# Kernel tuning notes

Measured on AMD Instinct MI355X. Metric: run time of the kernel, lower is better.

## Reference

```python
import jax, jax.numpy as jnp
import numpy as np

NEG_SLOPE = 0.2

def _gat_conv(x, W, att_src, att_dst, bias, src, dst, n_nodes):
    # x: [N, F_in], W: [F_in, F_out], att_*: [F_out], bias: [F_out]
    h = x @ W                                   # [N, F_out]
    a_src = h @ att_src                         # [N]
    a_dst = h @ att_dst                         # [N]
    e = a_src[src] + a_dst[dst]                 # [E]
    e = jnp.where(e > 0, e, NEG_SLOPE * e)      # LeakyReLU
    # segment softmax over incoming edges of each destination node
    m = jax.ops.segment_max(e, dst, num_segments=n_nodes)
    ex = jnp.exp(e - m[dst])
    denom = jax.ops.segment_sum(ex, dst, num_segments=n_nodes)
    alpha = ex / denom[dst]                     # [E]
    msg = alpha[:, None] * h[src]               # [E, F_out]
    out = jax.ops.segment_sum(msg, dst, num_segments=n_nodes)
    return out + bias

def setup_inputs() -> dict:
    key = jax.random.key(0)
    ks = jax.random.split(key, 12)
    N, E, F_in, H, F_out = 50000, 800000, 128, 128, 128
    def glorot(k, shape):
        lim = float(np.sqrt(6.0 / sum(shape))) if len(shape) > 1 else float(np.sqrt(6.0 / shape[0]))
        return jax.random.uniform(k, shape, jnp.float32, -lim, lim)
    return {
        "x": jax.random.normal(ks[0], (N, F_in), jnp.float32),
        "edge_index": jax.random.randint(ks[1], (2, E), 0, N, jnp.int64),
        "W1": glorot(ks[2], (F_in, H)),
        "att_src1": glorot(ks[3], (H,)),
        "att_dst1": glorot(ks[4], (H,)),
        "b1": jnp.zeros((H,), jnp.float32),
        "W2": glorot(ks[5], (H, F_out)),
        "att_src2": glorot(ks[6], (F_out,)),
        "att_dst2": glorot(ks[7], (F_out,)),
        "b2": jnp.zeros((F_out,), jnp.float32),
    }

def reference(x, edge_index, W1, att_src1, att_dst1, b1, W2, att_src2, att_dst2, b2):
    n_nodes = x.shape[0]
    # add self loops (PyG GATConv default)
    loops = jnp.arange(n_nodes, dtype=edge_index.dtype)
    src = jnp.concatenate([edge_index[0], loops])
    dst = jnp.concatenate([edge_index[1], loops])
    h = _gat_conv(x, W1, att_src1, att_dst1, b1, src, dst, n_nodes)
    h = jax.nn.relu(h)
    h = _gat_conv(h, W2, att_src2, att_dst2, b2, src, dst, n_nodes)
    return jax.nn.relu(h)
```

## Files before the change

### kernel.cpp

```cpp
#include <hip/hip_runtime.h>
#include <cstdint>

#define NEG_SLOPE 0.2f
#define F 128

#define BKT_SHIFT 7
#define BKT_SIZE  128
#define NBK_PAD   512
#define CHUNK     4096
#define EPT       8
#define CAP       3072

typedef unsigned short u16;
typedef unsigned int u32;
typedef float float8_t __attribute__((ext_vector_type(8)));
typedef float float4_t __attribute__((ext_vector_type(4)));
typedef short short8_t __attribute__((ext_vector_type(8)));

__device__ inline u16 f2bf(float f) {
    u32 u = __float_as_uint(f);
    u32 r = u + 0x7fffu + ((u >> 16) & 1u);
    return (u16)(r >> 16);
}
__device__ inline float bflo(u32 v) { return __uint_as_float(v << 16); }
__device__ inline float bfhi(u32 v) { return __uint_as_float(v & 0xffff0000u); }

__device__ inline void prep_unit(const float* __restrict__ W, u16* __restrict__ Wt, int u) {
    int frag = u >> 6, lane = u & 63;
    int K0 = frag >> 3, nt = frag & 7;
    int kbase = K0 * 32 + (lane >> 4) * 8;
    int n = nt * 16 + (lane & 15);
    u32 w[4];
    #pragma unroll
    for (int p = 0; p < 4; ++p) {
        u16 e0 = f2bf(W[(size_t)(kbase + 2 * p) * F + n]);
        u16 e1 = f2bf(W[(size_t)(kbase + 2 * p + 1) * F + n]);
        w[p] = (u32)e0 | ((u32)e1 << 16);
    }
    uint4 o; o.x = w[0]; o.y = w[1]; o.z = w[2]; o.w = w[3];
    ((uint4*)Wt)[u] = o;
}

__device__ inline int block_excl_scan_512(int v, int tid, int* wsum) {
    int incl = v;
    #pragma unroll
    for (int o = 1; o < 64; o <<= 1) {
        int u = __shfl_up(incl, o);
        if ((tid & 63) >= o) incl += u;
    }
    if ((tid & 63) == 63) wsum[tid >> 6] = incl;
    __syncthreads();
    int woff = 0;
    #pragma unroll
    for (int w0 = 0; w0 < 7; ++w0) woff += (w0 < (tid >> 6)) ? wsum[w0] : 0;
    return woff + incl - v;
}

__global__ void __launch_bounds__(512) scatter_prep_kernel(const int* __restrict__ ei, int E, int tot,
                                                           int* __restrict__ bucketCursor,
                                                           u32* __restrict__ pairs,
                                                           const float* __restrict__ W1, u16* __restrict__ Wt1,
                                                           const float* __restrict__ W2, u16* __restrict__ Wt2,
                                                           int nScatBlocks) {
    if ((int)blockIdx.x >= nScatBlocks) {
        int pb = blockIdx.x - nScatBlocks;
        int u = (pb & 3) * 512 + threadIdx.x;
        if (pb < 4) prep_unit(W1, Wt1, u);
        else        prep_unit(W2, Wt2, u);
        return;
    }
    __shared__ int hist[NBK_PAD], excl[NBK_PAD], lcur[NBK_PAD], runb[NBK_PAD];
    __shared__ int wsum[8];
    __shared__ u32 stage[CHUNK];
    __shared__ u16 bktid[CHUNK];
    int tid = threadIdx.x;
    hist[tid] = 0;
    __syncthreads();
    int base = blockIdx.x * CHUNK;
    int chunkCnt = min(CHUNK, tot - base);
    int rs[EPT], rd[EPT];
    int w = base + tid * EPT;
    if (w + EPT <= E) {
        int4 s0 = *(const int4*)&ei[w];
        int4 s1 = *(const int4*)&ei[w + 4];
        int4 d0 = *(const int4*)&ei[E + w];
        int4 d1 = *(const int4*)&ei[E + w + 4];
        rs[0] = s0.x; rs[1] = s0.y; rs[2] = s0.z; rs[3] = s0.w;
        rs[4] = s1.x; rs[5] = s1.y; rs[6] = s1.z; rs[7] = s1.w;
        rd[0] = d0.x; rd[1] = d0.y; rd[2] = d0.z; rd[3] = d0.w;
        rd[4] = d1.x; rd[5] = d1.y; rd[6] = d1.z; rd[7] = d1.w;
        #pragma unroll
        for (int i = 0; i < EPT; ++i) atomicAdd(&hist[rd[i] >> BKT_SHIFT], 1);
    } else {
        #pragma unroll
        for (int i = 0; i < EPT; ++i) {
            int e = w + i;
            rd[i] = -1;
            if (e < tot) {
                int s, d;
                if (e < E) { s = ei[e]; d = ei[E + e]; } else { s = e - E; d = s; }
                rs[i] = s; rd[i] = d;
                atomicAdd(&hist[d >> BKT_SHIFT], 1);
            }
        }
    }
    __syncthreads();
    int v = hist[tid];
    int ex = block_excl_scan_512(v, tid, wsum);
    excl[tid] = ex;
    lcur[tid] = ex;
    if (v > 0) runb[tid] = tid * CAP + atomicAdd(&bucketCursor[tid], v);
    __syncthreads();
    #pragma unroll
    for (int i = 0; i < EPT; ++i) {
        if (rd[i] >= 0) {
            int b = rd[i] >> BKT_SHIFT;
            int pos = atomicAdd(&lcur[b], 1);
            stage[pos] = ((u32)rs[i] << BKT_SHIFT) | (u32)(rd[i] & (BKT_SIZE - 1));
            bktid[pos] = (u16)b;
        }
    }
    __syncthreads();
    for (int j = tid; j < chunkCnt; j += 512) {
        int b = (int)bktid[j];
        size_t idx = (size_t)runb[b] + (j - excl[b]);
        if (idx < (size_t)(b + 1) * CAP)
            pairs[idx] = stage[j];
    }
}

__device__ void build_body(const u32* __restrict__ pairs, const int* __restrict__ bucketCursor,
                           int* __restrict__ row_ptr, int* __restrict__ csr,
                           int N, int tot, int b, char* smem) {
    u32* stage  = (u32*)smem;
    int* sorted = (int*)(smem + CAP * 4);
    int* hist   = (int*)(smem + CAP * 8);
    int* pfx    = (int*)(smem + CAP * 8 + 512);
    int* cur    = (int*)(smem + CAP * 8 + 1024);
    int* red    = (int*)(smem + CAP * 8 + 1536);
    int tid = threadIdx.x;

    int part = 0;
    for (int i = tid; i < b; i += 256) part += min(bucketCursor[i], CAP);
    #pragma unroll
    for (int o = 32; o > 0; o >>= 1) part += __shfl_xor(part, o);
    if ((tid & 63) == 0) red[tid >> 6] = part;
    if (tid < BKT_SIZE) hist[tid] = 0;
    __syncthreads();
    int dstb = red[0] + red[1] + red[2] + red[3];
    int cnt = min(bucketCursor[b], CAP);

    size_t srcb = (size_t)b * CAP;
    for (int j = tid; j < cnt; j += 256) {
        u32 p = pairs[srcb + j];
        stage[j] = p;
        atomicAdd(&hist[p & (BKT_SIZE - 1)], 1);
    }
    __syncthreads();
    if (tid < BKT_SIZE) pfx[tid] = hist[tid];
    __syncthreads();
    for (int o = 1; o < BKT_SIZE; o <<= 1) {
        int u = 0;
        if (tid < BKT_SIZE && tid >= o) u = pfx[tid - o];
        __syncthreads();
        if (tid < BKT_SIZE) pfx[tid] += u;
        __syncthreads();
    }
    if (tid < BKT_SIZE) {
        int ex = pfx[tid] - hist[tid];
        cur[tid] = ex;
        int d = b * BKT_SIZE + tid;
        if (d < N) row_ptr[d] = dstb + ex;
    }
    __syncthreads();
    for (int j = tid; j < cnt; j += 256) {
        u32 p = stage[j];
        int pos = atomicAdd(&cur[p & (BKT_SIZE - 1)], 1);
        sorted[pos] = (int)(p >> BKT_SHIFT);
    }
    __syncthreads();
    for (int j = tid; j < cnt; j += 256) csr[(size_t)dstb + j] = sorted[j];
    if (b == 0 && tid == 0) row_ptr[N] = tot;
}

template<int IN_BF16>
__device__ void gemm_body(const void* __restrict__ in, const u16* __restrict__ Wt,
                          const float* __restrict__ att_s, const float* __restrict__ att_d,
                          u16* __restrict__ h, float* __restrict__ asrc, float* __restrict__ adst,
                          int N, int gblk, u16* wlds) {
    int tid = threadIdx.x;
    {
        const uint4* src = (const uint4*)Wt;
        uint4* dst = (uint4*)wlds;
        #pragma unroll
        for (int i = 0; i < 8; ++i) dst[tid + i * 256] = src[tid + i * 256];
    }
    __syncthreads();
    int wave = tid >> 6, lane = tid & 63;
    int li = lane & 15, grp = lane >> 4;
    int rowBase = (gblk * 4 + wave) * 16;
    if (rowBase >= N) return;
    int row = rowBase + li;
    if (row > N - 1) row = N - 1;

    short8_t b[4];
    if (IN_BF16) {
        const u16* xp = (const u16*)in + (size_t)row * F + grp * 8;
        #pragma unroll
        for (int K0 = 0; K0 < 4; ++K0)
            b[K0] = *(const short8_t*)(xp + K0 * 32);
    } else {
        const float* xp = (const float*)in + (size_t)row * F + grp * 8;
        #pragma unroll
        for (int K0 = 0; K0 < 4; ++K0) {
            float8_t xv = *(const float8_t*)(xp + K0 * 32);
            short8_t t;
            #pragma unroll
            for (int i = 0; i < 8; ++i) t[i] = (short)f2bf(xv[i]);
            b[K0] = t;
        }
    }

    float4_t acc[8];
    #pragma unroll
    for (int nt = 0; nt < 8; ++nt) acc[nt] = (float4_t){0.f, 0.f, 0.f, 0.f};
    #pragma unroll
    for (int nt = 0; nt < 8; ++nt) {
        #pragma unroll
        for (int K0 = 0; K0 < 4; ++K0) {
            short8_t a = *(const short8_t*)&wlds[((K0 * 8 + nt) * 64 + lane) * 8];
            acc[nt] = __builtin_amdgcn_mfma_f32_16x16x32_bf16(a, b[K0], acc[nt], 0, 0, 0);
        }
    }

    u16* hr = h + (size_t)row * F + grp * 4;
    #pragma unroll
    for (int nt = 0; nt < 8; ++nt) {
        u32 lo = (u32)f2bf(acc[nt][0]) | ((u32)f2bf(acc[nt][1]) << 16);
        u32 hi = (u32)f2bf(acc[nt][2]) | ((u32)f2bf(acc[nt][3]) << 16);
        uint2 st; st.x = lo; st.y = hi;
        *(uint2*)(hr + (size_t)nt * 16) = st;
    }

    float rs = 0.f, rd = 0.f;
    #pragma unroll
    for (int nt = 0; nt < 8; ++nt) {
        float4 a4 = *(const float4*)(att_s + nt * 16 + grp * 4);
        float4 d4 = *(const float4*)(att_d + nt * 16 + grp * 4);
        rs += acc[nt][0] * a4.x + acc[nt][1] * a4.y + acc[nt][2] * a4.z + acc[nt][3] * a4.w;
        rd += acc[nt][0] * d4.x + acc[nt][1] * d4.y + acc[nt][2] * d4.z + acc[nt][3] * d4.w;
    }
    rs += __shfl_xor(rs, 16); rs += __shfl_xor(rs, 32);
    rd += __shfl_xor(rd, 16); rd += __shfl_xor(rd, 32);
    if (grp == 0) { asrc[row] = rs; adst[row] = rd; }
}

__global__ void __launch_bounds__(256) build_gemm_kernel(
    const u32* __restrict__ pairs, const int* __restrict__ bucketCursor,
    int* __restrict__ row_ptr, int* __restrict__ csr, int N, int tot,
    const float* __restrict__ x, const u16* __restrict__ Wt,
    const float* __restrict__ att_s, const float* __restrict__ att_d,
    u16* __restrict__ h, float* __restrict__ asrc, float* __restrict__ adst, int NBK)
{
    __shared__ __align__(16) char smem[32768];
    if ((int)blockIdx.x < NBK) {
        build_body(pairs, bucketCursor, row_ptr, csr, N, tot, blockIdx.x, smem);
    } else {
        gemm_body<0>(x, Wt, att_s, att_d, h, asrc, adst, N, blockIdx.x - NBK, (u16*)smem);
    }
}

__device__ __forceinline__ void rowfma(uint4 v, float pp, float (&acc)[8]) {
    acc[0] = fmaf(pp, bflo(v.x), acc[0]); acc[1] = fmaf(pp, bfhi(v.x), acc[1]);
    acc[2] = fmaf(pp, bflo(v.y), acc[2]); acc[3] = fmaf(pp, bfhi(v.y), acc[3]);
    acc[4] = fmaf(pp, bflo(v.z), acc[4]); acc[5] = fmaf(pp, bfhi(v.z), acc[5]);
    acc[6] = fmaf(pp, bflo(v.w), acc[6]); acc[7] = fmaf(pp, bfhi(v.w), acc[7]);
}

template<int U>
__device__ __forceinline__ void gfma(const uint4* __restrict__ h4, int lane, int s, float p, int t,
                                     float (&acc)[8]) {
    int ss[U]; float pp[U]; uint4 vv[U];
    #pragma unroll
    for (int i = 0; i < U; ++i) { ss[i] = __shfl(s, t + i, 16); pp[i] = __shfl(p, t + i, 16); }
    #pragma unroll
    for (int i = 0; i < U; ++i) vv[i] = h4[(size_t)ss[i] * 16 + lane];
    #pragma unroll
    for (int i = 0; i < U; ++i) rowfma(vv[i], pp[i], acc);
}

__device__ __forceinline__ float agg_core(
    const u16* __restrict__ h, const float* __restrict__ asrc, float ad,
    int start, int deg, const int* __restrict__ csr, int lane, float (&acc)[8]) {
    const uint4* h4 = (const uint4*)h;
    float denom = 0.f;
    int c0 = 0;
    int cnt = min(16, deg);
    int s = 0; float a = 0.f;
    if (lane < cnt) { s = csr[start + lane]; a = asrc[s]; }
    for (;;) {
        float p = 0.f;
        if (lane < cnt) {
            float e = a + ad;
            e = (e > 0.f) ? e : NEG_SLOPE * e;
            p = __expf(fminf(e, 70.f));
        }
        denom += p;

        int nc0 = c0 + 16;
        int ncnt = min(16, deg - nc0);
        int s2 = 0; float a2 = 0.f;
        if (nc0 < deg && lane < ncnt) { s2 = csr[start + nc0 + lane]; a2 = asrc[s2]; }

        int t = 0;
        for (; t + 8 <= cnt; t += 8) gfma<8>(h4, lane, s, p, t, acc);
        for (; t + 4 <= cnt; t += 4) gfma<4>(h4, lane, s, p, t, acc);
        for (; t < cnt; ++t)         gfma<1>(h4, lane, s, p, t, acc);

        if (nc0 >= deg) break;
        c0 = nc0; cnt = ncnt; s = s2; a = a2;
    }
    #pragma unroll
    for (int o = 1; o < 16; o <<= 1) denom += __shfl_xor(denom, o);
    return denom;
}

#define OL_STRIDE 136
__global__ void __launch_bounds__(256) agg_gemm_kernel(
    const u16* __restrict__ h, const float* __restrict__ asrc, const float* __restrict__ adst,
    const int* __restrict__ row_ptr, const int* __restrict__ csr,
    const float* __restrict__ bias,
    const u16* __restrict__ Wt2, const float* __restrict__ att_s2, const float* __restrict__ att_d2,
    u16* __restrict__ h2, float* __restrict__ asrc2, float* __restrict__ adst2, int N)
{
    __shared__ u16 out_lds[16 * OL_STRIDE];
    __shared__ float sdots[2][4][16];
    int tid = threadIdx.x;
    int gidBase = blockIdx.x * 16;
    int gid = gidBase + (tid >> 4);
    int lane = tid & 15;

    int start = row_ptr[gid];
    int deg = row_ptr[gid + 1] - start;
    float acc[8] = {0.f, 0.f, 0.f, 0.f, 0.f, 0.f, 0.f, 0.f};
    float denom = agg_core(h, asrc, adst[gid], start, deg, csr, lane, acc);
    float inv = 1.0f / denom;
    const float* bp = bias + lane * 8;
    u32 wpk[4];
    #pragma unroll
    for (int p2 = 0; p2 < 4; ++p2) {
        float v0 = fmaf(acc[2 * p2],     inv, bp[2 * p2]);
        float v1 = fmaf(acc[2 * p2 + 1], inv, bp[2 * p2 + 1]);
        v0 = v0 > 0.f ? v0 : 0.f;
        v1 = v1 > 0.f ? v1 : 0.f;
        wpk[p2] = (u32)f2bf(v0) | ((u32)f2bf(v1) << 16);
    }
    {
        uint4 st; st.x = wpk[0]; st.y = wpk[1]; st.z = wpk[2]; st.w = wpk[3];
        *(uint4*)&out_lds[(tid >> 4) * OL_STRIDE + lane * 8] = st;
    }
    __syncthreads();

    int l = tid & 63, wv = tid >> 6;
    int li = l & 15, grp = l >> 4;
    short8_t b[4];
    #pragma unroll
    for (int K0 = 0; K0 < 4; ++K0)
        b[K0] = *(const short8_t*)&out_lds[li * OL_STRIDE + grp * 8 + K0 * 32];

    float rs = 0.f, rd = 0.f;
    #pragma unroll
    for (int q = 0; q < 2; ++q) {
        int nt = wv * 2 + q;
        float4_t acc2 = (float4_t){0.f, 0.f, 0.f, 0.f};
        #pragma unroll
        for (int K0 = 0; K0 < 4; ++K0) {
            short8_t a = *(const short8_t*)&Wt2[((K0 * 8 + nt) * 64 + l) * 8];
            acc2 = __builtin_amdgcn_mfma_f32_16x16x32_bf16(a, b[K0], acc2, 0, 0, 0);
        }
        int row = gidBase + li;
        u32 lo = (u32)f2bf(acc2[0]) | ((u32)f2bf(acc2[1]) << 16);
        u32 hi = (u32)f2bf(acc2[2]) | ((u32)f2bf(acc2[3]) << 16);
        uint2 st; st.x = lo; st.y = hi;
        *(uint2*)(h2 + (size_t)row * F + nt * 16 + grp * 4) = st;
        float4 a4 = *(const float4*)(att_s2 + nt * 16 + grp * 4);
        float4 d4 = *(const float4*)(att_d2 + nt * 16 + grp * 4);
        rs += acc2[0] * a4.x + acc2[1] * a4.y + acc2[2] * a4.z + acc2[3] * a4.w;
        rd += acc2[0] * d4.x + acc2[1] * d4.y + acc2[2] * d4.z + acc2[3] * d4.w;
    }
    rs += __shfl_xor(rs, 16); rs += __shfl_xor(rs, 32);
    rd += __shfl_xor(rd, 16); rd += __shfl_xor(rd, 32);
    if (grp == 0) { sdots[0][wv][li] = rs; sdots[1][wv][li] = rd; }
    __syncthreads();
    if (tid < 16) {
        float s = sdots[0][0][tid] + sdots[0][1][tid] + sdots[0][2][tid] + sdots[0][3][tid];
        float d = sdots[1][0][tid] + sdots[1][1][tid] + sdots[1][2][tid] + sdots[1][3][tid];
        asrc2[gidBase + tid] = s;
        adst2[gidBase + tid] = d;
    }
}

__global__ void __launch_bounds__(256) aggregate_out_kernel(
    const u16* __restrict__ h, const float* __restrict__ asrc, const float* __restrict__ adst,
    const int* __restrict__ row_ptr, const int* __restrict__ csr,
    const float* __restrict__ bias, float* __restrict__ out, int N)
{
    int gid = blockIdx.x * 16 + (threadIdx.x >> 4);
    if (gid >= N) return;
    int lane = threadIdx.x & 15;
    int start = row_ptr[gid];
    int deg = row_ptr[gid + 1] - start;
    float acc[8] = {0.f, 0.f, 0.f, 0.f, 0.f, 0.f, 0.f, 0.f};
    float denom = agg_core(h, asrc, adst[gid], start, deg, csr, lane, acc);
    float inv = 1.0f / denom;
    const float* bp = bias + lane * 8;
    float r[8];
    #pragma unroll
    for (int j = 0; j < 8; ++j) {
        float v = fmaf(acc[j], inv, bp[j]);
        r[j] = v > 0.f ? v : 0.f;
    }
    float4 o0 = make_float4(r[0], r[1], r[2], r[3]);
    float4 o1 = make_float4(r[4], r[5], r[6], r[7]);
    ((float4*)out)[(size_t)gid * 32 + lane * 2]     = o0;
    ((float4*)out)[(size_t)gid * 32 + lane * 2 + 1] = o1;
}

static inline size_t align_up(size_t v, size_t a) { return (v + a - 1) & ~(a - 1); }

extern "C" void kernel_launch(void* const* d_in, const int* in_sizes, int n_in,
                              void* d_out, int out_size, void* d_ws, size_t ws_size,
                              hipStream_t stream) {
    const float* x   = (const float*)d_in[0];
    const int*   ei  = (const int*)d_in[1];
    const float* W1  = (const float*)d_in[2];
    const float* as1 = (const float*)d_in[3];
    const float* ad1 = (const float*)d_in[4];
    const float* b1  = (const float*)d_in[5];
    const float* W2  = (const float*)d_in[6];
    const float* as2 = (const float*)d_in[7];
    const float* ad2 = (const float*)d_in[8];
    const float* b2  = (const float*)d_in[9];

    int N = in_sizes[0] / F;
    int E = in_sizes[1] / 2;
    int tot = E + N;

    char* ws = (char*)d_ws;
    size_t off = 0;
    #define ALLOC(type, name, count)                                    \
        type* name = (type*)(ws + off);                                  \
        off = align_up(off + (size_t)(count) * sizeof(type), 256);
    ALLOC(u16,   h,       (size_t)N * F);
    ALLOC(u16,   h2,      (size_t)N * F);
    ALLOC(float, asrc,    N);
    ALLOC(float, adst,    N);
    ALLOC(float, asrc2,   N);
    ALLOC(float, adst2,   N);
    ALLOC(int,   row_ptr, N + 4);
    ALLOC(int,   csr,     tot);
    ALLOC(u32,   pairs,   (size_t)NBK_PAD * CAP);
    ALLOC(int,   bucketCursor, NBK_PAD);
    ALLOC(u16,   Wt1,     16384);
    ALLOC(u16,   Wt2,     16384);
    #undef ALLOC

    hipMemsetAsync(bucketCursor, 0, NBK_PAD * sizeof(int), stream);

    int NBK = (N + BKT_SIZE - 1) / BKT_SIZE;
    int nchunks = (tot + CHUNK - 1) / CHUNK;
    int ngemm = (N + 63) / 64;
    int nagg  = (N + 15) / 16;

    scatter_prep_kernel<<<nchunks + 8, 512, 0, stream>>>(ei, E, tot, bucketCursor, pairs,
                                                         W1, Wt1, W2, Wt2, nchunks);
    build_gemm_kernel<<<NBK + ngemm, 256, 0, stream>>>(pairs, bucketCursor, row_ptr, csr, N, tot,
                                                       x, Wt1, as1, ad1, h, asrc, adst, NBK);
    agg_gemm_kernel<<<nagg, 256, 0, stream>>>(h, asrc, adst, row_ptr, csr, b1,
                                              Wt2, as2, ad2, h2, asrc2, adst2, N);
    aggregate_out_kernel<<<nagg, 256, 0, stream>>>(h2, asrc2, adst2, row_ptr, csr, b2,
                                                   (float*)d_out, N);
}
```

Baseline: 187.2 us.

## Move layer-1 GEMM into scatter kernel and convert W1 per block in LDS

The first-layer GEMM (x@W1 plus attention logits) now runs in the same launch as the edge bucket scatter instead of sharing a launch with the CSR build. Each GEMM block converts W1 to bf16 fragments directly into LDS, which removes the separate Wt1 prep pass and lets the GEMM start without waiting on it. GEMM blocks grow to 512 threads covering 128 rows. The build kernel becomes a standalone launch. The tradeoff is that each GEMM block redoes the W1 conversion from global fp32, and the fused kernel's LDS footprint grows slightly.

After: 193.2 us. 1.03x slower.

```diff
diff --git a/kernel.cpp b/kernel.cpp
--- a/kernel.cpp
+++ b/kernel.cpp
@@ -25,7 +25,7 @@
 __device__ inline float bflo(u32 v) { return __uint_as_float(v << 16); }
 __device__ inline float bfhi(u32 v) { return __uint_as_float(v & 0xffff0000u); }
 
-__device__ inline void prep_unit(const float* __restrict__ W, u16* __restrict__ Wt, int u) {
+__device__ inline void prep_unit(const float* __restrict__ W, uint4* __restrict__ dst, int u) {
     int frag = u >> 6, lane = u & 63;
     int K0 = frag >> 3, nt = frag & 7;
     int kbase = K0 * 32 + (lane >> 4) * 8;
@@ -38,7 +38,7 @@
         w[p] = (u32)e0 | ((u32)e1 << 16);
     }
     uint4 o; o.x = w[0]; o.y = w[1]; o.z = w[2]; o.w = w[3];
-    ((uint4*)Wt)[u] = o;
+    dst[u] = o;
 }
 
 __device__ inline int block_excl_scan_512(int v, int tid, int* wsum) {
@@ -56,27 +56,20 @@
     return woff + incl - v;
 }
 
-__global__ void __launch_bounds__(512) scatter_prep_kernel(const int* __restrict__ ei, int E, int tot,
-                                                           int* __restrict__ bucketCursor,
-                                                           u32* __restrict__ pairs,
-                                                           const float* __restrict__ W1, u16* __restrict__ Wt1,
-                                                           const float* __restrict__ W2, u16* __restrict__ Wt2,
-                                                           int nScatBlocks) {
-    if ((int)blockIdx.x >= nScatBlocks) {
-        int pb = blockIdx.x - nScatBlocks;
-        int u = (pb & 3) * 512 + threadIdx.x;
-        if (pb < 4) prep_unit(W1, Wt1, u);
-        else        prep_unit(W2, Wt2, u);
-        return;
-    }
-    __shared__ int hist[NBK_PAD], excl[NBK_PAD], lcur[NBK_PAD], runb[NBK_PAD];
-    __shared__ int wsum[8];
-    __shared__ u32 stage[CHUNK];
-    __shared__ u16 bktid[CHUNK];
+__device__ void scatter_body(const int* __restrict__ ei, int E, int tot,
+                             int* __restrict__ bucketCursor, u32* __restrict__ pairs,
+                             int bid, char* smem) {
+    u32* stage = (u32*)smem;
+    u16* bktid = (u16*)(smem + 16384);
+    int* hist  = (int*)(smem + 24576);
+    int* excl  = (int*)(smem + 26624);
+    int* lcur  = (int*)(smem + 28672);
+    int* runb  = (int*)(smem + 30720);
+    int* wsum  = (int*)(smem + 32768);
     int tid = threadIdx.x;
     hist[tid] = 0;
     __syncthreads();
-    int base = blockIdx.x * CHUNK;
+    int base = bid * CHUNK;
     int chunkCnt = min(CHUNK, tot - base);
     int rs[EPT], rd[EPT];
     int w = base + tid * EPT;
@@ -129,16 +122,98 @@
     }
 }
 
-__device__ void build_body(const u32* __restrict__ pairs, const int* __restrict__ bucketCursor,
-                           int* __restrict__ row_ptr, int* __restrict__ csr,
-                           int N, int tot, int b, char* smem) {
+__device__ void gemm1_body(const float* __restrict__ x, const float* __restrict__ W,
+                           const float* __restrict__ att_s, const float* __restrict__ att_d,
+                           u16* __restrict__ h, float* __restrict__ asrc, float* __restrict__ adst,
+                           int N, int gblk, u16* wlds) {
+    int tid = threadIdx.x;
+    #pragma unroll
+    for (int i = 0; i < 4; ++i) prep_unit(W, (uint4*)wlds, tid + i * 512);
+    __syncthreads();
+    int wave = tid >> 6, lane = tid & 63;
+    int li = lane & 15, grp = lane >> 4;
+    int rowBase = (gblk * 8 + wave) * 16;
+    if (rowBase >= N) return;
+    int row = rowBase + li;
+    if (row > N - 1) row = N - 1;
+
+    short8_t b[4];
+    const float* xp = x + (size_t)row * F + grp * 8;
+    #pragma unroll
+    for (int K0 = 0; K0 < 4; ++K0) {
+        float8_t xv = *(const float8_t*)(xp + K0 * 32);
+        short8_t t;
+        #pragma unroll
+        for (int i = 0; i < 8; ++i) t[i] = (short)f2bf(xv[i]);
+        b[K0] = t;
+    }
+
+    float4_t acc[8];
+    #pragma unroll
+    for (int nt = 0; nt < 8; ++nt) acc[nt] = (float4_t){0.f, 0.f, 0.f, 0.f};
+    #pragma unroll
+    for (int nt = 0; nt < 8; ++nt) {
+        #pragma unroll
+        for (int K0 = 0; K0 < 4; ++K0) {
+            short8_t a = *(const short8_t*)&wlds[((K0 * 8 + nt) * 64 + lane) * 8];
+            acc[nt] = __builtin_amdgcn_mfma_f32_16x16x32_bf16(a, b[K0], acc[nt], 0, 0, 0);
+        }
+    }
+
+    u16* hr = h + (size_t)row * F + grp * 4;
+    #pragma unroll
+    for (int nt = 0; nt < 8; ++nt) {
+        u32 lo = (u32)f2bf(acc[nt][0]) | ((u32)f2bf(acc[nt][1]) << 16);
+        u32 hi = (u32)f2bf(acc[nt][2]) | ((u32)f2bf(acc[nt][3]) << 16);
+        uint2 st; st.x = lo; st.y = hi;
+        *(uint2*)(hr + (size_t)nt * 16) = st;
+    }
+
+    float rs = 0.f, rd = 0.f;
+    #pragma unroll
+    for (int nt = 0; nt < 8; ++nt) {
+        float4 a4 = *(const float4*)(att_s + nt * 16 + grp * 4);
+        float4 d4 = *(const float4*)(att_d + nt * 16 + grp * 4);
+        rs += acc[nt][0] * a4.x + acc[nt][1] * a4.y + acc[nt][2] * a4.z + acc[nt][3] * a4.w;
+        rd += acc[nt][0] * d4.x + acc[nt][1] * d4.y + acc[nt][2] * d4.z + acc[nt][3] * d4.w;
+    }
+    rs += __shfl_xor(rs, 16); rs += __shfl_xor(rs, 32);
+    rd += __shfl_xor(rd, 16); rd += __shfl_xor(rd, 32);
+    if (grp == 0) { asrc[row] = rs; adst[row] = rd; }
+}
+
+__global__ void __launch_bounds__(512) fused1_kernel(
+    const int* __restrict__ ei, int E, int tot,
+    int* __restrict__ bucketCursor, u32* __restrict__ pairs,
+    const float* __restrict__ W2, u16* __restrict__ Wt2,
+    const float* __restrict__ x, const float* __restrict__ W1,
+    const float* __restrict__ att_s, const float* __restrict__ att_d,
+    u16* __restrict__ h, float* __restrict__ asrc, float* __restrict__ adst,
+    int N, int nScat)
+{
+    __shared__ __align__(16) char smem[32800];
+    int bid = blockIdx.x;
+    if (bid < nScat) {
+        scatter_body(ei, E, tot, bucketCursor, pairs, bid, smem);
+    } else if (bid < nScat + 4) {
+        prep_unit(W2, (uint4*)Wt2, (bid - nScat) * 512 + threadIdx.x);
+    } else {
+        gemm1_body(x, W1, att_s, att_d, h, asrc, adst, N, bid - nScat - 4, (u16*)smem);
+    }
+}
+
+__global__ void __launch_bounds__(256) build_kernel(
+    const u32* __restrict__ pairs, const int* __restrict__ bucketCursor,
+    int* __restrict__ row_ptr, int* __restrict__ csr, int N, int tot)
+{
+    __shared__ __align__(16) char smem[26368];
     u32* stage  = (u32*)smem;
     int* sorted = (int*)(smem + CAP * 4);
     int* hist   = (int*)(smem + CAP * 8);
     int* pfx    = (int*)(smem + CAP * 8 + 512);
     int* cur    = (int*)(smem + CAP * 8 + 1024);
     int* red    = (int*)(smem + CAP * 8 + 1536);
-    int tid = threadIdx.x;
+    int b = blockIdx.x, tid = threadIdx.x;
 
     int part = 0;
     for (int i = tid; i < b; i += 256) part += min(bucketCursor[i], CAP);
@@ -181,93 +256,6 @@
     __syncthreads();
     for (int j = tid; j < cnt; j += 256) csr[(size_t)dstb + j] = sorted[j];
     if (b == 0 && tid == 0) row_ptr[N] = tot;
-}
-
-template<int IN_BF16>
-__device__ void gemm_body(const void* __restrict__ in, const u16* __restrict__ Wt,
-                          const float* __restrict__ att_s, const float* __restrict__ att_d,
-                          u16* __restrict__ h, float* __restrict__ asrc, float* __restrict__ adst,
-                          int N, int gblk, u16* wlds) {
-    int tid = threadIdx.x;
-    {
-        const uint4* src = (const uint4*)Wt;
-        uint4* dst = (uint4*)wlds;
-        #pragma unroll
-        for (int i = 0; i < 8; ++i) dst[tid + i * 256] = src[tid + i * 256];
-    }
-    __syncthreads();
-    int wave = tid >> 6, lane = tid & 63;
-    int li = lane & 15, grp = lane >> 4;
-    int rowBase = (gblk * 4 + wave) * 16;
-    if (rowBase >= N) return;
-    int row = rowBase + li;
-    if (row > N - 1) row = N - 1;
-
-    short8_t b[4];
-    if (IN_BF16) {
-        const u16* xp = (const u16*)in + (size_t)row * F + grp * 8;
-        #pragma unroll
-        for (int K0 = 0; K0 < 4; ++K0)
-            b[K0] = *(const short8_t*)(xp + K0 * 32);
-    } else {
-        const float* xp = (const float*)in + (size_t)row * F + grp * 8;
-        #pragma unroll
-        for (int K0 = 0; K0 < 4; ++K0) {
-            float8_t xv = *(const float8_t*)(xp + K0 * 32);
-            short8_t t;
-            #pragma unroll
-            for (int i = 0; i < 8; ++i) t[i] = (short)f2bf(xv[i]);
-            b[K0] = t;
-        }
-    }
-
-    float4_t acc[8];
-    #pragma unroll
-    for (int nt = 0; nt < 8; ++nt) acc[nt] = (float4_t){0.f, 0.f, 0.f, 0.f};
-    #pragma unroll
-    for (int nt = 0; nt < 8; ++nt) {
-        #pragma unroll
-        for (int K0 = 0; K0 < 4; ++K0) {
-            short8_t a = *(const short8_t*)&wlds[((K0 * 8 + nt) * 64 + lane) * 8];
-            acc[nt] = __builtin_amdgcn_mfma_f32_16x16x32_bf16(a, b[K0], acc[nt], 0, 0, 0);
-        }
-    }
-
-    u16* hr = h + (size_t)row * F + grp * 4;
-    #pragma unroll
-    for (int nt = 0; nt < 8; ++nt) {
-        u32 lo = (u32)f2bf(acc[nt][0]) | ((u32)f2bf(acc[nt][1]) << 16);
-        u32 hi = (u32)f2bf(acc[nt][2]) | ((u32)f2bf(acc[nt][3]) << 16);
-        uint2 st; st.x = lo; st.y = hi;
-        *(uint2*)(hr + (size_t)nt * 16) = st;
-    }
-
-    float rs = 0.f, rd = 0.f;
-    #pragma unroll
-    for (int nt = 0; nt < 8; ++nt) {
-        float4 a4 = *(const float4*)(att_s + nt * 16 + grp * 4);
-        float4 d4 = *(const float4*)(att_d + nt * 16 + grp * 4);
-        rs += acc[nt][0] * a4.x + acc[nt][1] * a4.y + acc[nt][2] * a4.z + acc[nt][3] * a4.w;
-        rd += acc[nt][0] * d4.x + acc[nt][1] * d4.y + acc[nt][2] * d4.z + acc[nt][3] * d4.w;
-    }
-    rs += __shfl_xor(rs, 16); rs += __shfl_xor(rs, 32);
-    rd += __shfl_xor(rd, 16); rd += __shfl_xor(rd, 32);
-    if (grp == 0) { asrc[row] = rs; adst[row] = rd; }
-}
-
-__global__ void __launch_bounds__(256) build_gemm_kernel(
-    const u32* __restrict__ pairs, const int* __restrict__ bucketCursor,
-    int* __restrict__ row_ptr, int* __restrict__ csr, int N, int tot,
-    const float* __restrict__ x, const u16* __restrict__ Wt,
-    const float* __restrict__ att_s, const float* __restrict__ att_d,
-    u16* __restrict__ h, float* __restrict__ asrc, float* __restrict__ adst, int NBK)
-{
-    __shared__ __align__(16) char smem[32768];
-    if ((int)blockIdx.x < NBK) {
-        build_body(pairs, bucketCursor, row_ptr, csr, N, tot, blockIdx.x, smem);
-    } else {
-        gemm_body<0>(x, Wt, att_s, att_d, h, asrc, adst, N, blockIdx.x - NBK, (u16*)smem);
-    }
 }
 
 __device__ __forceinline__ void rowfma(uint4 v, float pp, float (&acc)[8]) {
@@ -461,7 +449,6 @@
     ALLOC(int,   csr,     tot);
     ALLOC(u32,   pairs,   (size_t)NBK_PAD * CAP);
     ALLOC(int,   bucketCursor, NBK_PAD);
-    ALLOC(u16,   Wt1,     16384);
     ALLOC(u16,   Wt2,     16384);
     #undef ALLOC
 
@@ -469,13 +456,13 @@
 
     int NBK = (N + BKT_SIZE - 1) / BKT_SIZE;
     int nchunks = (tot + CHUNK - 1) / CHUNK;
-    int ngemm = (N + 63) / 64;
+    int ngemm = (N + 127) / 128;
     int nagg  = (N + 15) / 16;
 
-    scatter_prep_kernel<<<nchunks + 8, 512, 0, stream>>>(ei, E, tot, bucketCursor, pairs,
-                                                         W1, Wt1, W2, Wt2, nchunks);
-    build_gemm_kernel<<<NBK + ngemm, 256, 0, stream>>>(pairs, bucketCursor, row_ptr, csr, N, tot,
-                                                       x, Wt1, as1, ad1, h, asrc, adst, NBK);
+    fused1_kernel<<<nchunks + 4 + ngemm, 512, 0, stream>>>(ei, E, tot, bucketCursor, pairs,
+                                                           W2, Wt2, x, W1, as1, ad1,
+                                                           h, asrc, adst, N, nchunks);
+    build_kernel<<<NBK, 256, 0, stream>>>(pairs, bucketCursor, row_ptr, csr, N, tot);
     agg_gemm_kernel<<<nagg, 256, 0, stream>>>(h, asrc, adst, row_ptr, csr, b1,
                                               Wt2, as2, ad2, h2, asrc2, adst2, N);
     aggregate_out_kernel<<<nagg, 256, 0, stream>>>(h2, asrc2, adst2, row_ptr, csr, b2,
```

## Split final aggregation into alpha precompute and feature-sliced gather kernels

Applied to the files above, without the earlier changes.

Replaces the fused final aggregation kernel with two kernels. The first computes normalized attention coefficients per edge and writes them to a workspace array. The second does the weighted gather in eight 16-feature slices, with blocks interleaved by slice, so that concurrently running blocks touch a narrower part of h2 and get better cache locality. This costs an extra launch, an extra alpha write and read per edge, and a repeated csr/alpha read in every slice.

New measurement: 257.5 us. 37.6% more time.

```diff
diff --git a/kernel.cpp b/kernel.cpp
--- a/kernel.cpp
+++ b/kernel.cpp
@@ -400,30 +400,93 @@
     }
 }
 
-__global__ void __launch_bounds__(256) aggregate_out_kernel(
-    const u16* __restrict__ h, const float* __restrict__ asrc, const float* __restrict__ adst,
+__global__ void __launch_bounds__(256) alpha_kernel(
+    const float* __restrict__ asrc, const float* __restrict__ adst,
     const int* __restrict__ row_ptr, const int* __restrict__ csr,
-    const float* __restrict__ bias, float* __restrict__ out, int N)
+    float* __restrict__ alpha, int N)
 {
     int gid = blockIdx.x * 16 + (threadIdx.x >> 4);
     if (gid >= N) return;
     int lane = threadIdx.x & 15;
     int start = row_ptr[gid];
     int deg = row_ptr[gid + 1] - start;
-    float acc[8] = {0.f, 0.f, 0.f, 0.f, 0.f, 0.f, 0.f, 0.f};
-    float denom = agg_core(h, asrc, adst[gid], start, deg, csr, lane, acc);
+    float ad = adst[gid];
+    int d1 = min(deg, 16), d2 = min(deg - 16, 16);
+    float p1 = 0.f, p2 = 0.f;
+    if (lane < d1) {
+        float e = asrc[csr[start + lane]] + ad;
+        e = (e > 0.f) ? e : NEG_SLOPE * e;
+        p1 = __expf(fminf(e, 70.f));
+    }
+    if (lane < d2) {
+        float e = asrc[csr[start + 16 + lane]] + ad;
+        e = (e > 0.f) ? e : NEG_SLOPE * e;
+        p2 = __expf(fminf(e, 70.f));
+    }
+    float denom = p1 + p2;
+    for (int c0 = 32; c0 < deg; c0 += 16) {
+        float p = 0.f;
+        if (lane < min(16, deg - c0)) {
+            float e = asrc[csr[start + c0 + lane]] + ad;
+            e = (e > 0.f) ? e : NEG_SLOPE * e;
+            p = __expf(fminf(e, 70.f));
+            alpha[start + c0 + lane] = p;
+        }
+        denom += p;
+    }
+    #pragma unroll
+    for (int o = 1; o < 16; o <<= 1) denom += __shfl_xor(denom, o);
     float inv = 1.0f / denom;
-    const float* bp = bias + lane * 8;
-    float r[8];
-    #pragma unroll
-    for (int j = 0; j < 8; ++j) {
-        float v = fmaf(acc[j], inv, bp[j]);
-        r[j] = v > 0.f ? v : 0.f;
-    }
-    float4 o0 = make_float4(r[0], r[1], r[2], r[3]);
-    float4 o1 = make_float4(r[4], r[5], r[6], r[7]);
-    ((float4*)out)[(size_t)gid * 32 + lane * 2]     = o0;
-    ((float4*)out)[(size_t)gid * 32 + lane * 2 + 1] = o1;
+    if (lane < d1) alpha[start + lane] = p1 * inv;
+    if (lane < d2) alpha[start + 16 + lane] = p2 * inv;
+    for (int c0 = 32; c0 < deg; c0 += 16)
+        if (lane < min(16, deg - c0)) alpha[start + c0 + lane] *= inv;
+}
+
+__global__ void __launch_bounds__(256) agg_slice_kernel(
+    const u16* __restrict__ h2, const float* __restrict__ alpha,
+    const int* __restrict__ row_ptr, const int* __restrict__ csr,
+    const float* __restrict__ bias, float* __restrict__ out, int N)
+{
+    int slice = blockIdx.x & 7;
+    int chunk = blockIdx.x >> 3;
+    int grp = threadIdx.x >> 2;
+    int lane = threadIdx.x & 3;
+    int node = chunk * 64 + grp;
+    if (node >= N) return;
+    int start = row_ptr[node];
+    int deg = row_ptr[node + 1] - start;
+    const u16* hbase = h2 + (size_t)slice * 16 + lane * 4;
+    float a0 = 0.f, a1 = 0.f, a2 = 0.f, a3 = 0.f;
+    for (int c0 = 0; c0 < deg; c0 += 4) {
+        int cnt = min(4, deg - c0);
+        int s = 0; float al = 0.f;
+        if (lane < cnt) { s = csr[start + c0 + lane]; al = alpha[start + c0 + lane]; }
+        int s0 = __shfl(s, 0, 4), s1 = __shfl(s, 1, 4);
+        int s2 = __shfl(s, 2, 4), s3 = __shfl(s, 3, 4);
+        float w0 = __shfl(al, 0, 4), w1 = __shfl(al, 1, 4);
+        float w2 = __shfl(al, 2, 4), w3 = __shfl(al, 3, 4);
+        uint2 v0 = *(const uint2*)(hbase + (size_t)s0 * 128);
+        uint2 v1 = *(const uint2*)(hbase + (size_t)s1 * 128);
+        uint2 v2 = *(const uint2*)(hbase + (size_t)s2 * 128);
+        uint2 v3 = *(const uint2*)(hbase + (size_t)s3 * 128);
+        a0 = fmaf(w0, bflo(v0.x), a0); a1 = fmaf(w0, bfhi(v0.x), a1);
+        a2 = fmaf(w0, bflo(v0.y), a2); a3 = fmaf(w0, bfhi(v0.y), a3);
+        a0 = fmaf(w1, bflo(v1.x), a0); a1 = fmaf(w1, bfhi(v1.x), a1);
+        a2 = fmaf(w1, bflo(v1.y), a2); a3 = fmaf(w1, bfhi(v1.y), a3);
+        a0 = fmaf(w2, bflo(v2.x), a0); a1 = fmaf(w2, bfhi(v2.x), a1);
+        a2 = fmaf(w2, bflo(v2.y), a2); a3 = fmaf(w2, bfhi(v2.y), a3);
+        a0 = fmaf(w3, bflo(v3.x), a0); a1 = fmaf(w3, bfhi(v3.x), a1);
+        a2 = fmaf(w3, bflo(v3.y), a2); a3 = fmaf(w3, bfhi(v3.y), a3);
+    }
+    float4 bv = *(const float4*)(bias + slice * 16 + lane * 4);
+    float4 o;
+    o.x = a0 + bv.x; o.y = a1 + bv.y; o.z = a2 + bv.z; o.w = a3 + bv.w;
+    o.x = o.x > 0.f ? o.x : 0.f;
+    o.y = o.y > 0.f ? o.y : 0.f;
+    o.z = o.z > 0.f ? o.z : 0.f;
+    o.w = o.w > 0.f ? o.w : 0.f;
+    *(float4*)(out + (size_t)node * F + slice * 16 + lane * 4) = o;
 }
 
 static inline size_t align_up(size_t v, size_t a) { return (v + a - 1) & ~(a - 1); }
@@ -459,6 +522,7 @@
     ALLOC(float, adst2,   N);
     ALLOC(int,   row_ptr, N + 4);
     ALLOC(int,   csr,     tot);
+    ALLOC(float, alpha,   tot);
     ALLOC(u32,   pairs,   (size_t)NBK_PAD * CAP);
     ALLOC(int,   bucketCursor, NBK_PAD);
     ALLOC(u16,   Wt1,     16384);
@@ -471,6 +535,7 @@
     int nchunks = (tot + CHUNK - 1) / CHUNK;
     int ngemm = (N + 63) / 64;
     int nagg  = (N + 15) / 16;
+    int nslc  = ((N + 63) / 64) * 8;
 
     scatter_prep_kernel<<<nchunks + 8, 512, 0, stream>>>(ei, E, tot, bucketCursor, pairs,
                                                          W1, Wt1, W2, Wt2, nchunks);
@@ -478,6 +543,6 @@
                                                        x, Wt1, as1, ad1, h, asrc, adst, NBK);
     agg_gemm_kernel<<<nagg, 256, 0, stream>>>(h, asrc, adst, row_ptr, csr, b1,
                                               Wt2, as2, ad2, h2, asrc2, adst2, N);
-    aggregate_out_kernel<<<nagg, 256, 0, stream>>>(h2, asrc2, adst2, row_ptr, csr, b2,
-                                                   (float*)d_out, N);
-}
+    alpha_kernel<<<nagg, 256, 0, stream>>>(asrc2, adst2, row_ptr, csr, alpha, N);
+    agg_slice_kernel<<<nslc, 256, 0, stream>>>(h2, alpha, row_ptr, csr, b2, (float*)d_out, N);
+}
```
